# Performance work log

Measured on AMD Instinct MI355X. Metric: run time of the kernel, lower is better.

The kernel has to match this reference:

```python
import jax, jax.numpy as jnp
import numpy as np

B, MB, NB, C = 4, 4096, 16384, 64

def setup_inputs() -> dict:
    key = jax.random.key(0)
    k1, k2, k3 = jax.random.split(key, 3)
    xyz = jax.random.normal(k1, (B * MB, 3), dtype=jnp.float32) * 10.0
    new_xyz = jax.random.normal(k2, (B * NB, 3), dtype=jnp.float32) * 10.0
    features = jax.random.normal(k3, (B * MB, C), dtype=jnp.float32)
    xyz_batch_cnt = jnp.full((B,), MB, dtype=jnp.int32)
    new_xyz_batch_cnt = jnp.full((B,), NB, dtype=jnp.int32)
    return {
        "xyz": xyz,
        "xyz_batch_cnt": xyz_batch_cnt,
        "new_xyz": new_xyz,
        "new_xyz_batch_cnt": new_xyz_batch_cnt,
        "features": features,
    }

def _three_nn_interp(query, known, feats):
    # query: (Nb,3), known: (Mb,3), feats: (Mb,C)
    # squared pairwise distances (Nb, Mb)
    d2 = (jnp.sum(query * query, -1, keepdims=True)
          - 2.0 * (query @ known.T)
          + jnp.sum(known * known, -1)[None, :])
    neg_d2, idx = jax.lax.top_k(-d2, 3)            # 3 nearest, (Nb,3)
    dist = jnp.sqrt(jnp.maximum(-neg_d2, 0.0))      # OpenPCDet returns sqrt(dist2)
    dist_recip = 1.0 / (dist + 1e-8)
    weight = dist_recip / jnp.sum(dist_recip, -1, keepdims=True)  # (Nb,3)
    gathered = feats[idx]                           # (Nb,3,C)
    return jnp.einsum('nkc,nk->nc', gathered, weight)

def reference(xyz, xyz_batch_cnt, new_xyz, new_xyz_batch_cnt, features):
    b = xyz_batch_cnt.shape[0]
    mb = xyz.shape[0] // b
    nb = new_xyz.shape[0] // b
    known_b = xyz.reshape(b, mb, 3)
    query_b = new_xyz.reshape(b, nb, 3)
    feats_b = features.reshape(b, mb, -1)
    out = jax.vmap(_three_nn_interp)(query_b, known_b, feats_b)  # (B,Nb,C)
    return out.reshape(b * nb, -1)
```

## Files before the change

### kernel.cpp

```cpp
#include <hip/hip_runtime.h>
#include <math.h>

#define NBIN   512
#define BEXT   64.0f
#define WSLACK 0.02f
#define AWIN   4.0f
#define BTH1   1024

__device__ __forceinline__ int bin1(float x) {
    int c = (int)floorf((x + BEXT) * 4.0f);
    return min(NBIN - 1, max(0, c));
}
__device__ __forceinline__ unsigned f2sort(float f) {
    int b = __float_as_int(f);
    return (unsigned)b ^ (0x80000000u | (unsigned)(b >> 31));
}
__device__ __forceinline__ float sort2f(unsigned u) {
    unsigned b = (u & 0x80000000u) ? (u ^ 0x80000000u) : ~u;
    return __uint_as_float(b);
}
__device__ __forceinline__ void ins3k(unsigned long long k,
                                      unsigned long long& k0,
                                      unsigned long long& k1,
                                      unsigned long long& k2) {
    const bool c0 = k < k0, c1 = k < k1, c2 = k < k2;
    k2 = c1 ? k1 : (c2 ? k : k2);
    k1 = c0 ? k0 : (c1 ? k : k1);
    k0 = c0 ? k  : k0;
}
__device__ __forceinline__ unsigned long long shfl_xor_u64(unsigned long long v, int m) {
    unsigned lo = (unsigned)v, hi = (unsigned)(v >> 32);
    lo = __shfl_xor((int)lo, m, 64);
    hi = __shfl_xor((int)hi, m, 64);
    return ((unsigned long long)hi << 32) | lo;
}

extern "C" __global__ void __launch_bounds__(BTH1)
build1d(const float* __restrict__ xyz, const float* __restrict__ nxyz,
        int mb, int nb,
        float4* __restrict__ ps, int* __restrict__ pidx,
        int* __restrict__ qord, int* __restrict__ boff,
        int* __restrict__ ovf_cnt)
{
    __shared__ int hist[NBIN];
    __shared__ int scanb[NBIN];
    const int B    = (int)gridDim.x / 2;
    const bool isQ = (int)blockIdx.x >= B;
    const int b    = isQ ? (int)blockIdx.x - B : (int)blockIdx.x;
    const int tid  = threadIdx.x;
    const int n    = isQ ? nb : mb;
    const float* P = (isQ ? nxyz : xyz) + (size_t)b * n * 3;

    if (blockIdx.x == 0 && tid < B) ovf_cnt[tid] = 0;

    if (tid < NBIN) hist[tid] = 0;
    __syncthreads();
    for (int i = tid; i < n; i += BTH1) atomicAdd(&hist[bin1(P[i * 3])], 1);
    __syncthreads();
    int h = 0;
    if (tid < NBIN) { h = hist[tid]; scanb[tid] = h; }
    __syncthreads();
    for (int off = 1; off < NBIN; off <<= 1) {
        int t = 0;
        if (tid < NBIN && tid >= off) t = scanb[tid - off];
        __syncthreads();
        if (tid < NBIN) scanb[tid] += t;
        __syncthreads();
    }
    if (tid < NBIN) {
        const int excl = scanb[tid] - h;
        if (!isQ) {
            boff[(size_t)b * (NBIN + 1) + tid] = excl;
            if (tid == NBIN - 1) boff[(size_t)b * (NBIN + 1) + NBIN] = n;
        }
        hist[tid] = excl;
    }
    __syncthreads();
    for (int i = tid; i < n; i += BTH1) {
        const float x = P[i * 3], y = P[i * 3 + 1], z = P[i * 3 + 2];
        const int c = bin1(x);
        const int pos = atomicAdd(&hist[c], 1);
        if (isQ) {
            qord[(size_t)b * nb + pos] = i;
        } else {
            float pn;
            {
#pragma clang fp contract(off)
                pn = (x * x + y * y) + z * z;
            }
            ps[(size_t)b * mb + pos]   = make_float4(x, y, z, pn);
            pidx[(size_t)b * mb + pos] = i;
        }
    }
}

#define QWA  8
#define SWA  8
#define WVBA 4
#define WTHA (WVBA * 64)
#define QPBA (WVBA * QWA)
#define CHA  64

extern "C" __global__ void __launch_bounds__(WTHA)
knn_phaseA(const float* __restrict__ nxyz, const float* __restrict__ feats,
           const int* __restrict__ qord, const int* __restrict__ boff,
           const float4* __restrict__ ps, const int* __restrict__ pidx,
           float* __restrict__ out, int* __restrict__ ovf, float* __restrict__ ovf_ub,
           int* __restrict__ ovf_cnt, int mb, int nb, int C)
{
    __shared__ float4 sP[WVBA][CHA];
    __shared__ int    sI[WVBA][CHA];

    const int tid  = threadIdx.x;
    const int w    = tid >> 6;
    const int l    = tid & 63;
    const int qi   = l & 7;
    const int side = l >> 3;
    const int wid  = blockIdx.x * WVBA + w;
    const int q0   = wid * QWA;
    const int b    = q0 / nb;

    const int qloc = qord[q0 + qi];
    const int row  = b * nb + qloc;
    const float qx = nxyz[(size_t)row * 3 + 0];
    const float qy = nxyz[(size_t)row * 3 + 1];
    const float qz = nxyz[(size_t)row * 3 + 2];
    float qq;
    {
#pragma clang fp contract(off)
        qq = (qx * qx + qy * qy) + qz * qz;
    }

    float mn = qx, mx = qx;
#pragma unroll
    for (int m = 1; m < 64; m <<= 1) {
        mn = fminf(mn, __shfl_xor(mn, m, 64));
        mx = fmaxf(mx, __shfl_xor(mx, m, 64));
    }

    const int*    boffb = boff + (size_t)b * (NBIN + 1);
    const float4* psb   = ps   + (size_t)b * mb;
    const int*    pib   = pidx + (size_t)b * mb;

    unsigned long long k0 = ~0ull, k1 = ~0ull, k2 = ~0ull;

    float4 rP;
    int    rI = 0;
    bool   rV = false;
    auto issue = [&](int base, int hi) {
        const int cand = base + l;
        rV = cand < hi;
        if (rV) { rP = psb[cand]; rI = pib[cand]; }
    };
    auto commit = [&]() {
        if (rV) { sP[w][l] = rP; sI[w][l] = rI; }
    };
    auto process = [&](int cnt) {
#pragma unroll
        for (int u = 0; u < CHA / SWA; ++u) {
            const int j = side + u * SWA;
            if (j < cnt) {
                const float4 Pt = sP[w][j];
                const int    pi = sI[w][j];
                const float dot = fmaf(qz, Pt.z, fmaf(qy, Pt.y, qx * Pt.x));
                const float d2  = fmaf(-2.0f, dot, qq) + Pt.w;
                const unsigned long long key =
                    ((unsigned long long)f2sort(d2) << 32) | (unsigned)pi;
                if (key < k2) {
                    const bool c0 = key < k0, c1 = key < k1;
                    k2 = c1 ? k1 : key;
                    k1 = c0 ? k0 : (c1 ? key : k1);
                    k0 = c0 ? key : k0;
                }
            }
        }
    };

    const int blo = bin1(mn - AWIN);
    const int bhi = bin1(mx + AWIN);
    {
        const int lo = boffb[blo], hi = boffb[bhi + 1];
        if (lo < hi) {
            issue(lo, hi);
            for (int base = lo; base < hi; base += CHA) {
                commit();
                if (base + CHA < hi) issue(base + CHA, hi);
                process(min(CHA, hi - base));
            }
        }
    }

    unsigned long long m0 = k0, m1 = k1, m2 = k2;
#pragma unroll
    for (int mk = 8; mk <= 32; mk <<= 1) {
        const unsigned long long t0 = shfl_xor_u64(m0, mk);
        const unsigned long long t1 = shfl_xor_u64(m1, mk);
        const unsigned long long t2 = shfl_xor_u64(m2, mk);
        ins3k(t0, m0, m1, m2); ins3k(t1, m0, m1, m2); ins3k(t2, m0, m1, m2);
    }

    const unsigned h2 = (unsigned)(m2 >> 32);
    const float ub = (h2 == 0xFFFFFFFFu) ? INFINITY : sort2f(h2);
    const float eL = fmaf(0.25f, (float)blo, -BEXT);
    const float eR = fmaf(0.25f, (float)(bhi + 1), -BEXT);
    const float gL = qx - eL;
    const float gR = eR - qx;
    const bool okL = (blo == 0)        || (gL * gL > ub + WSLACK);
    const bool okR = (bhi >= NBIN - 1) || (gR * gR > ub + WSLACK);
    const bool resolved = okL && okR && (h2 != 0xFFFFFFFFu);

    const bool need = (side == 0) && !resolved;
    const unsigned long long bm = __ballot(need);
    if (bm) {
        const int rank = __popcll(bm & ((1ull << l) - 1ull));
        const int tot  = __popcll(bm);
        const int lead = __ffsll((unsigned long long)bm) - 1;
        int base = 0;
        if (l == lead) base = atomicAdd(&ovf_cnt[b], tot);
        base = __shfl(base, lead, 64);
        if (need) {
            ovf[(size_t)b * nb + base + rank]    = row;
            ovf_ub[(size_t)b * nb + base + rank] = ub;
        }
    }

    const float d0  = sort2f((unsigned)(m0 >> 32));
    const float d1  = sort2f((unsigned)(m1 >> 32));
    const float d2v = sort2f((unsigned)(m2 >> 32));
    const float da = sqrtf(fmaxf(d0, 0.0f));
    const float db = sqrtf(fmaxf(d1, 0.0f));
    const float dc = sqrtf(fmaxf(d2v, 0.0f));
    const float ra = 1.0f / (da + 1e-8f);
    const float rb = 1.0f / (db + 1e-8f);
    const float rc = 1.0f / (dc + 1e-8f);
    float rs;
    {
#pragma clang fp contract(off)
        rs = (ra + rb) + rc;
    }
    const float wa = ra / rs, wb = rb / rs, wc = rc / rs;
    const int   ia = b * mb + (int)(unsigned)(m0 & 0xFFFFFFFFu);
    const int   ib = b * mb + (int)(unsigned)(m1 & 0xFFFFFFFFu);
    const int   ic = b * mb + (int)(unsigned)(m2 & 0xFFFFFFFFu);

    for (int q = 0; q < QWA; ++q) {
        if (__shfl((int)resolved, q, 64) == 0) continue;
        const float wa_ = __shfl(wa, q, 64);
        const float wb_ = __shfl(wb, q, 64);
        const float wc_ = __shfl(wc, q, 64);
        const int   ia_ = __shfl(ia, q, 64);
        const int   ib_ = __shfl(ib, q, 64);
        const int   ic_ = __shfl(ic, q, 64);
        const int   rw_ = __shfl(row, q, 64);
        const size_t ga = (size_t)ia_ * C;
        const size_t gb = (size_t)ib_ * C;
        const size_t gc = (size_t)ic_ * C;
        const size_t go = (size_t)rw_ * C;
        for (int ch = l; ch < C; ch += 64) {
            out[go + ch] = wa_ * feats[ga + ch] + wb_ * feats[gb + ch] + wc_ * feats[gc + ch];
        }
    }
}

#define WPBB 8
#define BTH2 (WPBB * 64)

extern "C" __global__ void __launch_bounds__(BTH2)
knn_phaseB2(const float* __restrict__ nxyz, const float* __restrict__ feats,
            const int* __restrict__ ovf, const float* __restrict__ ovf_ub,
            const int* __restrict__ ovf_cnt, const int* __restrict__ boff,
            const float4* __restrict__ ps, const int* __restrict__ pidx,
            float* __restrict__ out, int mb, int nb, int C)
{
    const int tid  = threadIdx.x;
    const int w    = tid >> 6;
    const int l    = tid & 63;
    const int bpb  = nb / WPBB;
    const int bb   = (int)blockIdx.x / bpb;
    const int slot = ((int)blockIdx.x % bpb) * WPBB + w;
    const int cnt  = ovf_cnt[bb];
    if (slot >= cnt) return;

    const int   row = ovf[(size_t)bb * nb + slot];
    const float ub  = ovf_ub[(size_t)bb * nb + slot];
    const float qx = nxyz[(size_t)row * 3 + 0];
    const float qy = nxyz[(size_t)row * 3 + 1];
    const float qz = nxyz[(size_t)row * 3 + 2];
    float qq;
    {
#pragma clang fp contract(off)
        qq = (qx * qx + qy * qy) + qz * qz;
    }

    int blo = 0, bhi = NBIN - 1;
    if (ub < 1e30f) {
        const float r = sqrtf(ub + 2.0f * WSLACK);
        blo = bin1(qx - r);
        bhi = bin1(qx + r);
    }
    const int*    boffb = boff + (size_t)bb * (NBIN + 1);
    const float4* psb   = ps   + (size_t)bb * mb;
    const int*    pib   = pidx + (size_t)bb * mb;
    const int lo = boffb[blo], hi = boffb[bhi + 1];

    unsigned long long k0 = ~0ull, k1 = ~0ull, k2 = ~0ull;
#pragma unroll 4
    for (int t = lo + l; t < hi; t += 64) {
        const float4 Pt = psb[t];
        const int    pi = pib[t];
        const float dot = fmaf(qz, Pt.z, fmaf(qy, Pt.y, qx * Pt.x));
        const float d2  = fmaf(-2.0f, dot, qq) + Pt.w;
        const unsigned long long key =
            ((unsigned long long)f2sort(d2) << 32) | (unsigned)pi;
        if (key < k2) {
            const bool c0 = key < k0, c1 = key < k1;
            k2 = c1 ? k1 : key;
            k1 = c0 ? k0 : (c1 ? key : k1);
            k0 = c0 ? key : k0;
        }
    }

#pragma unroll
    for (int m = 1; m < 64; m <<= 1) {
        const unsigned long long t0 = shfl_xor_u64(k0, m);
        const unsigned long long t1 = shfl_xor_u64(k1, m);
        const unsigned long long t2 = shfl_xor_u64(k2, m);
        ins3k(t0, k0, k1, k2); ins3k(t1, k0, k1, k2); ins3k(t2, k0, k1, k2);
    }

    const float d0  = sort2f((unsigned)(k0 >> 32));
    const float d1  = sort2f((unsigned)(k1 >> 32));
    const float d2v = sort2f((unsigned)(k2 >> 32));
    const float da = sqrtf(fmaxf(d0, 0.0f));
    const float db = sqrtf(fmaxf(d1, 0.0f));
    const float dc = sqrtf(fmaxf(d2v, 0.0f));
    const float ra = 1.0f / (da + 1e-8f);
    const float rb = 1.0f / (db + 1e-8f);
    const float rc = 1.0f / (dc + 1e-8f);
    float rs;
    {
#pragma clang fp contract(off)
        rs = (ra + rb) + rc;
    }
    const float wa = ra / rs, wb = rb / rs, wc = rc / rs;
    const size_t ga = (size_t)(bb * mb + (int)(unsigned)(k0 & 0xFFFFFFFFu)) * C;
    const size_t gb = (size_t)(bb * mb + (int)(unsigned)(k1 & 0xFFFFFFFFu)) * C;
    const size_t gc = (size_t)(bb * mb + (int)(unsigned)(k2 & 0xFFFFFFFFu)) * C;
    const size_t go = (size_t)row * C;
    for (int ch = l; ch < C; ch += 64) {
        out[go + ch] = wa * feats[ga + ch] + wb * feats[gb + ch] + wc * feats[gc + ch];
    }
}

#define THREADS 512
#define WAVES   8
#define RQ      2
#define QPB     128
#define CHUNK   2048

extern "C" __global__ void __launch_bounds__(THREADS)
knn3_v5(const float* __restrict__ xyz,
        const float* __restrict__ new_xyz,
        const float* __restrict__ feats,
        float* __restrict__ out,
        int mb, int nb, int C)
{
    extern __shared__ float smem[];
    float4* s_pts = (float4*)smem;
    const int tid = threadIdx.x;
    const int w   = tid >> 6;
    const int l   = tid & 63;
    const int block_q0 = blockIdx.x * QPB;
    const int batch    = block_q0 / nb;
    const int known0   = batch * mb;

    float qx[RQ], qy[RQ], qz[RQ], qq[RQ];
#pragma unroll
    for (int r = 0; r < RQ; ++r) {
        const int gq = block_q0 + r * 64 + l;
        qx[r] = new_xyz[(size_t)gq * 3 + 0];
        qy[r] = new_xyz[(size_t)gq * 3 + 1];
        qz[r] = new_xyz[(size_t)gq * 3 + 2];
        {
#pragma clang fp contract(off)
            qq[r] = (qx[r] * qx[r] + qy[r] * qy[r]) + qz[r] * qz[r];
        }
    }
    float b0[RQ], b1[RQ], b2[RQ];
    int   i0[RQ], i1[RQ], i2[RQ];
#pragma unroll
    for (int r = 0; r < RQ; ++r) {
        b0[r] = INFINITY; b1[r] = INFINITY; b2[r] = INFINITY;
        i0[r] = 0; i1[r] = 0; i2[r] = 0;
    }
    const int nch = (mb + CHUNK - 1) / CHUNK;
    for (int c = 0; c < nch; ++c) {
        const int base = c * CHUNK;
        const int cnt  = min(CHUNK, mb - base);
        if (c > 0) __syncthreads();
        const float* src = xyz + (size_t)(known0 + base) * 3;
        for (int p = tid; p < cnt; p += THREADS) {
            const float px = src[p * 3 + 0];
            const float py = src[p * 3 + 1];
            const float pz = src[p * 3 + 2];
            float pn;
            {
#pragma clang fp contract(off)
                pn = (px * px + py * py) + pz * pz;
            }
            s_pts[p] = make_float4(px, py, pz, pn);
        }
        __syncthreads();
        const int lo = (w * cnt) / WAVES;
        const int hi = ((w + 1) * cnt) / WAVES;
#pragma unroll 4
        for (int p = lo; p < hi; ++p) {
            const float4 P = s_pts[p];
            const int gp = base + p;
#pragma unroll
            for (int r = 0; r < RQ; ++r) {
                const float dot = fmaf(qz[r], P.z, fmaf(qy[r], P.y, qx[r] * P.x));
                const float d2  = fmaf(-2.0f, dot, qq[r]) + P.w;
                const bool c0 = d2 < b0[r];
                const bool c1 = d2 < b1[r];
                const bool c2 = d2 < b2[r];
                const float n0 = fminf(d2, b0[r]);
                const float n1 = __builtin_amdgcn_fmed3f(d2, b0[r], b1[r]);
                const float n2 = __builtin_amdgcn_fmed3f(d2, b1[r], b2[r]);
                const int  j0 = c0 ? gp : i0[r];
                const int  j1 = c0 ? i0[r] : (c1 ? gp : i1[r]);
                const int  j2 = c1 ? i1[r] : (c2 ? gp : i2[r]);
                b0[r] = n0; b1[r] = n1; b2[r] = n2;
                i0[r] = j0; i1[r] = j1; i2[r] = j2;
            }
        }
    }
    __syncthreads();
    float* sB  = smem;
    int*   sI  = (int*)smem + 3 * WAVES * QPB;
    float* sFW = smem + 6 * WAVES * QPB;
    int*   sFI = (int*)sFW + 3 * QPB;
#pragma unroll
    for (int r = 0; r < RQ; ++r) {
        const int qb = r * 64 + l;
        sB[(0 * WAVES + w) * QPB + qb] = b0[r];
        sB[(1 * WAVES + w) * QPB + qb] = b1[r];
        sB[(2 * WAVES + w) * QPB + qb] = b2[r];
        sI[(0 * WAVES + w) * QPB + qb] = i0[r];
        sI[(1 * WAVES + w) * QPB + qb] = i1[r];
        sI[(2 * WAVES + w) * QPB + qb] = i2[r];
    }
    __syncthreads();
    if (tid < QPB) {
        float mv0 = sB[(0 * WAVES) * QPB + tid];
        float mv1 = sB[(1 * WAVES) * QPB + tid];
        float mv2 = sB[(2 * WAVES) * QPB + tid];
        int   mi0 = sI[(0 * WAVES) * QPB + tid];
        int   mi1 = sI[(1 * WAVES) * QPB + tid];
        int   mi2 = sI[(2 * WAVES) * QPB + tid];
        for (int c = 1; c < WAVES; ++c) {
#pragma unroll
            for (int kk = 0; kk < 3; ++kk) {
                const float x  = sB[(kk * WAVES + c) * QPB + tid];
                const int   xi = sI[(kk * WAVES + c) * QPB + tid];
                const bool c0 = (x < mv0) || (x == mv0 && xi < mi0);
                const bool c1 = (x < mv1) || (x == mv1 && xi < mi1);
                const bool c2 = (x < mv2) || (x == mv2 && xi < mi2);
                const float n2 = c1 ? mv1 : (c2 ? x : mv2);
                const int   j2 = c1 ? mi1 : (c2 ? xi : mi2);
                const float n1 = c0 ? mv0 : (c1 ? x : mv1);
                const int   j1 = c0 ? mi0 : (c1 ? xi : mi1);
                const float n0 = c0 ? x : mv0;
                const int   j0 = c0 ? xi : mi0;
                mv0 = n0; mv1 = n1; mv2 = n2;
                mi0 = j0; mi1 = j1; mi2 = j2;
            }
        }
        const float da = sqrtf(fmaxf(mv0, 0.0f));
        const float db = sqrtf(fmaxf(mv1, 0.0f));
        const float dc = sqrtf(fmaxf(mv2, 0.0f));
        const float ra = 1.0f / (da + 1e-8f);
        const float rb = 1.0f / (db + 1e-8f);
        const float rc = 1.0f / (dc + 1e-8f);
        float rsum;
        {
#pragma clang fp contract(off)
            rsum = (ra + rb) + rc;
        }
        sFW[0 * QPB + tid] = ra / rsum;
        sFW[1 * QPB + tid] = rb / rsum;
        sFW[2 * QPB + tid] = rc / rsum;
        sFI[0 * QPB + tid] = known0 + mi0;
        sFI[1 * QPB + tid] = known0 + mi1;
        sFI[2 * QPB + tid] = known0 + mi2;
    }
    __syncthreads();
    const int qpw = QPB / WAVES;
    for (int j = 0; j < qpw; ++j) {
        const int qi2 = w * qpw + j;
        const float wa = sFW[0 * QPB + qi2];
        const float wb = sFW[1 * QPB + qi2];
        const float wc = sFW[2 * QPB + qi2];
        const size_t ga = (size_t)sFI[0 * QPB + qi2] * C;
        const size_t gb = (size_t)sFI[1 * QPB + qi2] * C;
        const size_t gc = (size_t)sFI[2 * QPB + qi2] * C;
        const size_t go = (size_t)(block_q0 + qi2) * C;
        for (int ch = l; ch < C; ch += 64) {
            out[go + ch] = wa * feats[ga + ch] + wb * feats[gb + ch] + wc * feats[gc + ch];
        }
    }
}

#define FQPB 256
extern "C" __global__ void __launch_bounds__(FQPB)
knn3_fallback(const float* __restrict__ xyz,
              const float* __restrict__ new_xyz,
              const float* __restrict__ feats,
              float* __restrict__ out,
              int mb, int nb, int C)
{
    extern __shared__ float4 s_pts[];
    const int tid      = threadIdx.x;
    const int block_q0 = blockIdx.x * FQPB;
    const int batch    = block_q0 / nb;
    const int known0   = batch * mb;
    for (int p = tid; p < mb; p += FQPB) {
        const float px = xyz[(size_t)(known0 + p) * 3 + 0];
        const float py = xyz[(size_t)(known0 + p) * 3 + 1];
        const float pz = xyz[(size_t)(known0 + p) * 3 + 2];
        float pn;
        {
#pragma clang fp contract(off)
            pn = (px * px + py * py) + pz * pz;
        }
        s_pts[p] = make_float4(px, py, pz, pn);
    }
    __syncthreads();
    const int gq = block_q0 + tid;
    const float qx = new_xyz[(size_t)gq * 3 + 0];
    const float qy = new_xyz[(size_t)gq * 3 + 1];
    const float qz = new_xyz[(size_t)gq * 3 + 2];
    float qq;
    {
#pragma clang fp contract(off)
        qq = (qx * qx + qy * qy) + qz * qz;
    }
    float b0 = INFINITY, b1 = INFINITY, b2 = INFINITY;
    int   i0 = 0, i1 = 0, i2 = 0;
#pragma unroll 8
    for (int p = 0; p < mb; ++p) {
        const float4 P = s_pts[p];
        const float dot = fmaf(qz, P.z, fmaf(qy, P.y, qx * P.x));
        const float d2  = fmaf(-2.0f, dot, qq) + P.w;
        const bool c0 = d2 < b0;
        const bool c1 = d2 < b1;
        const bool c2 = d2 < b2;
        b2 = c1 ? b1 : (c2 ? d2 : b2);
        i2 = c1 ? i1 : (c2 ? p  : i2);
        b1 = c0 ? b0 : (c1 ? d2 : b1);
        i1 = c0 ? i0 : (c1 ? p  : i1);
        b0 = c0 ? d2 : b0;
        i0 = c0 ? p  : i0;
    }
    const float da = sqrtf(fmaxf(b0, 0.0f));
    const float db = sqrtf(fmaxf(b1, 0.0f));
    const float dc = sqrtf(fmaxf(b2, 0.0f));
    const float ra = 1.0f / (da + 1e-8f);
    const float rb = 1.0f / (db + 1e-8f);
    const float rc = 1.0f / (dc + 1e-8f);
    float rsum;
    {
#pragma clang fp contract(off)
        rsum = (ra + rb) + rc;
    }
    const float wa = ra / rsum, wb = rb / rsum, wc = rc / rsum;
    const size_t ga = (size_t)(known0 + i0) * C;
    const size_t gb = (size_t)(known0 + i1) * C;
    const size_t gc = (size_t)(known0 + i2) * C;
    const size_t go = (size_t)gq * C;
    for (int ch = 0; ch < C; ++ch) {
        out[go + ch] = wa * feats[ga + ch] + wb * feats[gb + ch] + wc * feats[gc + ch];
    }
}

extern "C" void kernel_launch(void* const* d_in, const int* in_sizes, int n_in,
                              void* d_out, int out_size, void* d_ws, size_t ws_size,
                              hipStream_t stream) {
    const float* xyz     = (const float*)d_in[0];
    const float* new_xyz = (const float*)d_in[2];
    const float* feats   = (const float*)d_in[4];
    float*       out     = (float*)d_out;

    const int n_known = in_sizes[0] / 3;
    const int B       = in_sizes[1];
    const int n_query = in_sizes[2] / 3;
    const int C       = in_sizes[4] / n_known;
    const int mb      = n_known / B;
    const int nb      = n_query / B;

    char* wp = (char*)d_ws;
    float4* ps      = (float4*)wp;  wp += (size_t)B * mb * sizeof(float4);
    int*    pidx    = (int*)wp;     wp += (size_t)B * mb * sizeof(int);
    int*    qord    = (int*)wp;     wp += (size_t)B * nb * sizeof(int);
    int*    boff    = (int*)wp;     wp += (size_t)B * (NBIN + 1) * sizeof(int);
    int*    ovf     = (int*)wp;     wp += (size_t)B * nb * sizeof(int);
    float*  ovf_ub  = (float*)wp;   wp += (size_t)B * nb * sizeof(float);
    int*    ovf_cnt = (int*)wp;     wp += (size_t)B * sizeof(int);
    const size_t need = (size_t)(wp - (char*)d_ws);

    if (ws_size >= need && (nb % QWA) == 0 && (n_query % QPBA) == 0 &&
        (nb % WPBB) == 0 && mb >= 3 && B <= BTH1) {
        build1d<<<2 * B, BTH1, 0, stream>>>(xyz, new_xyz, mb, nb, ps, pidx, qord,
                                            boff, ovf_cnt);
        knn_phaseA<<<n_query / QPBA, WTHA, 0, stream>>>(
            new_xyz, feats, qord, boff, ps, pidx, out, ovf, ovf_ub, ovf_cnt,
            mb, nb, C);
        knn_phaseB2<<<B * (nb / WPBB), BTH2, 0, stream>>>(
            new_xyz, feats, ovf, ovf_ub, ovf_cnt, boff, ps, pidx, out, mb, nb, C);
    } else if ((nb % QPB) == 0) {
        const size_t smem_chunk = (size_t)CHUNK * sizeof(float4);
        const size_t smem_merge = (size_t)(6 * WAVES * QPB + 6 * QPB) * sizeof(float);
        const size_t shmem = smem_chunk > smem_merge ? smem_chunk : smem_merge;
        knn3_v5<<<n_query / QPB, THREADS, shmem, stream>>>(
            xyz, new_xyz, feats, out, mb, nb, C);
    } else {
        const size_t shmem = (size_t)mb * sizeof(float4);
        knn3_fallback<<<(n_query + FQPB - 1) / FQPB, FQPB, shmem, stream>>>(
            xyz, new_xyz, feats, out, mb, nb, C);
    }
}
```

Baseline: 96.13 us.

## Split bin build into grid-wide kernels, prune candidates, narrow search window

Replaces the single per-batch build kernel, which ran only 2*B blocks, with four grid-wide kernels for zeroing, histogram, scan and scatter, using global atomics so the binning work spreads across the whole GPU. Phase A now pads chunks with infinite-distance sentinels so the per-candidate bounds check goes away, and it keeps a running third-best distance so most candidates are rejected before a key is built. The search window AWIN shrinks from 4 to 3, which scans fewer candidates but may send more queries to the overflow pass. The cost is three extra kernel launches, contended global atomics, and scatter order that is no longer deterministic within a bin.

```diff
diff --git a/kernel.cpp b/kernel.cpp
--- a/kernel.cpp
+++ b/kernel.cpp
@@ -4,8 +4,7 @@
 #define NBIN   512
 #define BEXT   64.0f
 #define WSLACK 0.02f
-#define AWIN   4.0f
-#define BTH1   1024
+#define AWIN   3.0f
 
 __device__ __forceinline__ int bin1(float x) {
     int c = (int)floorf((x + BEXT) * 4.0f);
@@ -35,61 +34,85 @@
     return ((unsigned long long)hi << 32) | lo;
 }
 
-extern "C" __global__ void __launch_bounds__(BTH1)
-build1d(const float* __restrict__ xyz, const float* __restrict__ nxyz,
-        int mb, int nb,
-        float4* __restrict__ ps, int* __restrict__ pidx,
-        int* __restrict__ qord, int* __restrict__ boff,
-        int* __restrict__ ovf_cnt)
-{
-    __shared__ int hist[NBIN];
-    __shared__ int scanb[NBIN];
-    const int B    = (int)gridDim.x / 2;
+extern "C" __global__ void __launch_bounds__(256)
+k_zero(int* __restrict__ bhistP, int* __restrict__ bhistQ,
+       int* __restrict__ ovf_cnt, int B)
+{
+    const int n = B * NBIN;
+    for (int i = blockIdx.x * 256 + threadIdx.x; i < n; i += gridDim.x * 256) {
+        bhistP[i] = 0; bhistQ[i] = 0;
+    }
+    if (blockIdx.x == 0 && (int)threadIdx.x < B) ovf_cnt[threadIdx.x] = 0;
+}
+
+extern "C" __global__ void __launch_bounds__(256)
+k_hist(const float* __restrict__ xyz, const float* __restrict__ nxyz,
+       int B, int mb, int nb,
+       int* __restrict__ bhistP, int* __restrict__ bhistQ)
+{
+    const int np = B * mb, tot = np + B * nb;
+    for (int i = blockIdx.x * 256 + threadIdx.x; i < tot; i += gridDim.x * 256) {
+        if (i < np) {
+            const int b = i / mb;
+            atomicAdd(&bhistP[b * NBIN + bin1(xyz[(size_t)i * 3])], 1);
+        } else {
+            const int j = i - np;
+            const int b = j / nb;
+            atomicAdd(&bhistQ[b * NBIN + bin1(nxyz[(size_t)j * 3])], 1);
+        }
+    }
+}
+
+extern "C" __global__ void __launch_bounds__(NBIN)
+k_scan(int* __restrict__ bhistP, int* __restrict__ bhistQ,
+       int* __restrict__ boff, int B, int mb)
+{
+    __shared__ int s[NBIN];
     const bool isQ = (int)blockIdx.x >= B;
     const int b    = isQ ? (int)blockIdx.x - B : (int)blockIdx.x;
-    const int tid  = threadIdx.x;
-    const int n    = isQ ? nb : mb;
-    const float* P = (isQ ? nxyz : xyz) + (size_t)b * n * 3;
-
-    if (blockIdx.x == 0 && tid < B) ovf_cnt[tid] = 0;
-
-    if (tid < NBIN) hist[tid] = 0;
-    __syncthreads();
-    for (int i = tid; i < n; i += BTH1) atomicAdd(&hist[bin1(P[i * 3])], 1);
-    __syncthreads();
-    int h = 0;
-    if (tid < NBIN) { h = hist[tid]; scanb[tid] = h; }
+    int* h = (isQ ? bhistQ : bhistP) + (size_t)b * NBIN;
+    const int tid = threadIdx.x;
+    const int v = h[tid];
+    s[tid] = v;
     __syncthreads();
     for (int off = 1; off < NBIN; off <<= 1) {
-        int t = 0;
-        if (tid < NBIN && tid >= off) t = scanb[tid - off];
+        const int t = (tid >= off) ? s[tid - off] : 0;
         __syncthreads();
-        if (tid < NBIN) scanb[tid] += t;
+        s[tid] += t;
         __syncthreads();
     }
-    if (tid < NBIN) {
-        const int excl = scanb[tid] - h;
-        if (!isQ) {
-            boff[(size_t)b * (NBIN + 1) + tid] = excl;
-            if (tid == NBIN - 1) boff[(size_t)b * (NBIN + 1) + NBIN] = n;
-        }
-        hist[tid] = excl;
-    }
-    __syncthreads();
-    for (int i = tid; i < n; i += BTH1) {
-        const float x = P[i * 3], y = P[i * 3 + 1], z = P[i * 3 + 2];
-        const int c = bin1(x);
-        const int pos = atomicAdd(&hist[c], 1);
-        if (isQ) {
-            qord[(size_t)b * nb + pos] = i;
-        } else {
+    const int excl = s[tid] - v;
+    h[tid] = excl;
+    if (!isQ) {
+        boff[(size_t)b * (NBIN + 1) + tid] = excl;
+        if (tid == NBIN - 1) boff[(size_t)b * (NBIN + 1) + NBIN] = mb;
+    }
+}
+
+extern "C" __global__ void __launch_bounds__(256)
+k_scat(const float* __restrict__ xyz, const float* __restrict__ nxyz,
+       int B, int mb, int nb,
+       int* __restrict__ bhistP, int* __restrict__ bhistQ,
+       float4* __restrict__ ps, int* __restrict__ pidx, int* __restrict__ qord)
+{
+    const int np = B * mb, tot = np + B * nb;
+    for (int i = blockIdx.x * 256 + threadIdx.x; i < tot; i += gridDim.x * 256) {
+        if (i < np) {
+            const int b = i / mb, li = i - b * mb;
+            const float x = xyz[(size_t)i * 3], y = xyz[(size_t)i * 3 + 1], z = xyz[(size_t)i * 3 + 2];
+            const int pos = atomicAdd(&bhistP[b * NBIN + bin1(x)], 1);
             float pn;
             {
 #pragma clang fp contract(off)
                 pn = (x * x + y * y) + z * z;
             }
             ps[(size_t)b * mb + pos]   = make_float4(x, y, z, pn);
-            pidx[(size_t)b * mb + pos] = i;
+            pidx[(size_t)b * mb + pos] = li;
+        } else {
+            const int j = i - np;
+            const int b = j / nb, li = j - b * nb;
+            const int pos = atomicAdd(&bhistQ[b * NBIN + bin1(nxyz[(size_t)j * 3])], 1);
+            qord[(size_t)b * nb + pos] = li;
         }
     }
 }
@@ -143,6 +166,7 @@
     const int*    pib   = pidx + (size_t)b * mb;
 
     unsigned long long k0 = ~0ull, k1 = ~0ull, k2 = ~0ull;
+    float d2keep = INFINITY;
 
     float4 rP;
     int    rI = 0;
@@ -153,25 +177,23 @@
         if (rV) { rP = psb[cand]; rI = pib[cand]; }
     };
     auto commit = [&]() {
-        if (rV) { sP[w][l] = rP; sI[w][l] = rI; }
+        sP[w][l] = rV ? rP : make_float4(0.0f, 0.0f, 0.0f, INFINITY);
+        sI[w][l] = rV ? rI : 0;
     };
-    auto process = [&](int cnt) {
+    auto process_chunk = [&]() {
 #pragma unroll
         for (int u = 0; u < CHA / SWA; ++u) {
             const int j = side + u * SWA;
-            if (j < cnt) {
-                const float4 Pt = sP[w][j];
-                const int    pi = sI[w][j];
-                const float dot = fmaf(qz, Pt.z, fmaf(qy, Pt.y, qx * Pt.x));
-                const float d2  = fmaf(-2.0f, dot, qq) + Pt.w;
+            const float4 Pt = sP[w][j];
+            const float dot = fmaf(qz, Pt.z, fmaf(qy, Pt.y, qx * Pt.x));
+            const float d2  = fmaf(-2.0f, dot, qq) + Pt.w;
+            if (d2 <= d2keep) {
+                const int pi = sI[w][j];
                 const unsigned long long key =
                     ((unsigned long long)f2sort(d2) << 32) | (unsigned)pi;
-                if (key < k2) {
-                    const bool c0 = key < k0, c1 = key < k1;
-                    k2 = c1 ? k1 : key;
-                    k1 = c0 ? k0 : (c1 ? key : k1);
-                    k0 = c0 ? key : k0;
-                }
+                ins3k(key, k0, k1, k2);
+                const unsigned h = (unsigned)(k2 >> 32);
+                d2keep = (h == 0xFFFFFFFFu) ? INFINITY : sort2f(h);
             }
         }
     };
@@ -185,7 +207,7 @@
             for (int base = lo; base < hi; base += CHA) {
                 commit();
                 if (base + CHA < hi) issue(base + CHA, hi);
-                process(min(CHA, hi - base));
+                process_chunk();
             }
         }
     }
@@ -200,14 +222,15 @@
     }
 
     const unsigned h2 = (unsigned)(m2 >> 32);
-    const float ub = (h2 == 0xFFFFFFFFu) ? INFINITY : sort2f(h2);
+    const bool have3 = (h2 != 0xFFFFFFFFu);
+    const float ub = have3 ? sort2f(h2) : INFINITY;
     const float eL = fmaf(0.25f, (float)blo, -BEXT);
     const float eR = fmaf(0.25f, (float)(bhi + 1), -BEXT);
     const float gL = qx - eL;
     const float gR = eR - qx;
     const bool okL = (blo == 0)        || (gL * gL > ub + WSLACK);
     const bool okR = (bhi >= NBIN - 1) || (gR * gR > ub + WSLACK);
-    const bool resolved = okL && okR && (h2 != 0xFFFFFFFFu);
+    const bool resolved = okL && okR && have3 && (ub < 1e30f);
 
     const bool need = (side == 0) && !resolved;
     const unsigned long long bm = __ballot(need);
@@ -606,12 +629,17 @@
     int*    ovf     = (int*)wp;     wp += (size_t)B * nb * sizeof(int);
     float*  ovf_ub  = (float*)wp;   wp += (size_t)B * nb * sizeof(float);
     int*    ovf_cnt = (int*)wp;     wp += (size_t)B * sizeof(int);
+    int*    bhistP  = (int*)wp;     wp += (size_t)B * NBIN * sizeof(int);
+    int*    bhistQ  = (int*)wp;     wp += (size_t)B * NBIN * sizeof(int);
     const size_t need = (size_t)(wp - (char*)d_ws);
 
     if (ws_size >= need && (nb % QWA) == 0 && (n_query % QPBA) == 0 &&
-        (nb % WPBB) == 0 && mb >= 3 && B <= BTH1) {
-        build1d<<<2 * B, BTH1, 0, stream>>>(xyz, new_xyz, mb, nb, ps, pidx, qord,
-                                            boff, ovf_cnt);
+        (nb % WPBB) == 0 && mb >= 3 && B <= 256) {
+        k_zero<<<64, 256, 0, stream>>>(bhistP, bhistQ, ovf_cnt, B);
+        k_hist<<<256, 256, 0, stream>>>(xyz, new_xyz, B, mb, nb, bhistP, bhistQ);
+        k_scan<<<2 * B, NBIN, 0, stream>>>(bhistP, bhistQ, boff, B, mb);
+        k_scat<<<256, 256, 0, stream>>>(xyz, new_xyz, B, mb, nb, bhistP, bhistQ,
+                                        ps, pidx, qord);
         knn_phaseA<<<n_query / QPBA, WTHA, 0, stream>>>(
             new_xyz, feats, qord, boff, ps, pidx, out, ovf, ovf_ub, ovf_cnt,
             mb, nb, C);
```

Measured after the change: 167.9 us. +74.7%, slower.
